# Performance work log

Hardware: AMD Instinct MI355X
Metric: run time of the kernel (lower is better)

Reference implementation:

```python
import jax, jax.numpy as jnp
import numpy as np

N, E, FS = 50000, 400000, 256
H, D = 8, 64            # GAT heads, hidden_size (per-head out_feats)
NH, DK, DV = 8, 64, 64  # transformer MHA
B = 1024
NEG_SLOPE = 0.2
EPS = 1e-6


def _layer_norm(x, g, b, eps=EPS):
    mu = x.mean(-1, keepdims=True)
    var = x.var(-1, keepdims=True)
    return (x - mu) / jnp.sqrt(var + eps) * g + b


def setup_inputs() -> dict:
    key = jax.random.key(0)
    ks = jax.random.split(key, 20)
    s = 0.02
    return {
        "features": jax.random.normal(ks[0], (N, FS), jnp.float32),
        "src": jax.random.randint(ks[1], (E,), 0, N, jnp.int32),
        "dst": jax.random.randint(ks[2], (E,), 0, N, jnp.int32),
        "url": jax.random.randint(ks[3], (B,), 1, N + 1, jnp.int32),  # 1-based ids
        # GATConv params (DGL-style)
        "gat_fc_w": jax.random.normal(ks[4], (FS, H * D), jnp.float32) * s,
        "attn_l": jax.random.normal(ks[5], (H, D), jnp.float32) * s,
        "attn_r": jax.random.normal(ks[6], (H, D), jnp.float32) * s,
        "gat_res_w": jax.random.normal(ks[7], (FS, H * D), jnp.float32) * s,
        "gat_bias": jnp.zeros((H, D), jnp.float32),
        # post-GAT LayerNorm
        "ln_g": jnp.ones((D,), jnp.float32),
        "ln_b": jnp.zeros((D,), jnp.float32),
        # MultiHeadAttention params
        "wq": jax.random.normal(ks[8], (D, NH * DK), jnp.float32) * s,
        "wk": jax.random.normal(ks[9], (D, NH * DK), jnp.float32) * s,
        "wv": jax.random.normal(ks[10], (D, NH * DV), jnp.float32) * s,
        "fc_w": jax.random.normal(ks[11], (NH * DV, D), jnp.float32) * s,
        "fc_b": jnp.zeros((D,), jnp.float32),
        "mha_ln_g": jnp.ones((D,), jnp.float32),
        "mha_ln_b": jnp.zeros((D,), jnp.float32),
        # final classifier
        "out_w": jax.random.normal(ks[12], (D, 2), jnp.float32) * s,
        "out_b": jnp.zeros((2,), jnp.float32),
    }


def reference(features, src, dst, url, gat_fc_w, attn_l, attn_r, gat_res_w,
              gat_bias, ln_g, ln_b, wq, wk, wv, fc_w, fc_b, mha_ln_g,
              mha_ln_b, out_w, out_b):
    # ---- GATConv (residual=True, bias, negative_slope=0.2, no activation) ----
    feat = (features @ gat_fc_w).reshape(N, H, D)          # [N,H,D]
    el = jnp.einsum('nhd,hd->nh', feat, attn_l)            # [N,H]
    er = jnp.einsum('nhd,hd->nh', feat, attn_r)            # [N,H]
    e = jax.nn.leaky_relu(el[src] + er[dst], NEG_SLOPE)    # [E,H] edge scores
    # segment softmax over incoming edges of each dst node
    m = jax.ops.segment_max(e, dst, num_segments=N)        # [N,H]
    m = jnp.where(jnp.isfinite(m), m, 0.0)
    ex = jnp.exp(e - m[dst])                               # [E,H]
    denom = jax.ops.segment_sum(ex, dst, num_segments=N)   # [N,H]
    a = ex / jnp.maximum(denom[dst], 1e-20)                # [E,H]
    msg = feat[src] * a[:, :, None]                        # [E,H,D]
    rst = jax.ops.segment_sum(msg, dst, num_segments=N)    # [N,H,D]
    res = (features @ gat_res_w).reshape(N, H, D)
    gat_emb = rst + res + gat_bias                         # [N,H,D]

    # ---- select batch nodes (url is 1-based) ----
    ids = url - 1
    x = gat_emb[ids]                                       # [B,H,D]
    x = _layer_norm(x, ln_g, ln_b)

    # ---- dense multi-head self-attention over the H gat heads (seq dim) ----
    residual = x
    q = (x @ wq).reshape(B, H, NH, DK)
    k = (x @ wk).reshape(B, H, NH, DK)
    v = (x @ wv).reshape(B, H, NH, DV)
    attn = jnp.einsum('bqhd,bkhd->bhqk', q, k) / jnp.sqrt(jnp.float32(DK))
    attn = jax.nn.softmax(attn, axis=-1)
    o = jnp.einsum('bhqk,bkhd->bqhd', attn, v).reshape(B, H, NH * DV)
    o = o @ fc_w + fc_b                                    # [B,H,D]
    o = _layer_norm(o + residual, mha_ln_g, mha_ln_b)

    # ---- pool + classify ----
    pooled = o.sum(axis=1)                                 # [B,D]
    logits = pooled @ out_w + out_b                        # [B,2]
    return logits
```

## Files before the change

### kernel.cpp

```cpp
#include <hip/hip_runtime.h>
#include <math.h>

#define Nn 50000
#define Ee 400000
#define FSz 256
#define HD_ 512
#define Bb 1024
#define HSZ 2048

static __device__ __forceinline__ int clampi(int v, int lo, int hi){
    return v < lo ? lo : (v > hi ? hi : v);
}
static __device__ __forceinline__ unsigned short f2bf(float f){
    unsigned int u = __float_as_uint(f);
    unsigned int r = u + 0x7FFFu + ((u >> 16) & 1u);
    return (unsigned short)(r >> 16);
}
static __device__ __forceinline__ float bflo(unsigned int v){ return __uint_as_float(v << 16); }
static __device__ __forceinline__ float bfhi(unsigned int v){ return __uint_as_float(v & 0xFFFF0000u); }

__global__ __launch_bounds__(256) void k_scatter(const int* __restrict__ src, const int* __restrict__ dst,
                                                 const int* __restrict__ url,
                                                 int* __restrict__ fill, int* __restrict__ slist,
                                                 const float* __restrict__ W,
                                                 const float* __restrict__ al,
                                                 const float* __restrict__ ar,
                                                 float* __restrict__ wl, float* __restrict__ wr){
    int t = threadIdx.x;
    if(blockIdx.x >= 1563){
        int bi = blockIdx.x - 1563;
        int wv = t >> 6, lane = t & 63;
        #pragma unroll
        for(int r = 0; r < 4; r++){
            int f = bi*16 + wv*4 + r;
            float pl[8], pr[8];
            #pragma unroll
            for(int h = 0; h < 8; h++){
                float w = W[f*512 + h*64 + lane];
                pl[h] = w * al[h*64 + lane];
                pr[h] = w * ar[h*64 + lane];
            }
            #pragma unroll
            for(int h = 0; h < 8; h++){
                #pragma unroll
                for(int m = 32; m >= 1; m >>= 1){
                    pl[h] += __shfl_xor(pl[h], m, 64);
                    pr[h] += __shfl_xor(pr[h], m, 64);
                }
            }
            #pragma unroll
            for(int h = 0; h < 8; h++){
                if(lane == h){ wl[h*256 + f] = pl[h]; wr[h*256 + f] = pr[h]; }
            }
        }
        return;
    }
    __shared__ int key[HSZ];
    __shared__ int chainhead[HSZ];
    __shared__ short nxt[Bb];
    for(int i = t; i < HSZ; i += 256){ key[i] = -1; chainhead[i] = -1; }
    __syncthreads();
    for(int b = t; b < Bb; b += 256){
        int n = clampi(url[b] - 1, 0, Nn - 1);
        int h = n & (HSZ - 1);
        while(true){
            int prev = atomicCAS(&key[h], -1, n);
            if(prev == -1 || prev == n) break;
            h = (h + 1) & (HSZ - 1);
        }
        int old = atomicExch(&chainhead[h], b);
        nxt[b] = (short)old;
    }
    __syncthreads();
    int e = blockIdx.x * 256 + t;
    if(e >= Ee) return;
    int d = dst[e];
    if((unsigned)d >= (unsigned)Nn) return;
    int h = d & (HSZ - 1);
    while(true){
        int k = key[h];
        if(k == -1) return;
        if(k == d) break;
        h = (h + 1) & (HSZ - 1);
    }
    int s = clampi(src[e], 0, Nn - 1);
    for(int b = chainhead[h]; b != -1; b = nxt[b]){
        int pos = atomicAdd(&fill[b], 1);
        if(pos < 64) slist[b*64 + pos] = s;
    }
}

__global__ __launch_bounds__(256) void k_gat(const float* __restrict__ features,
                                             const float* __restrict__ Wfc,
                                             const float* __restrict__ Wres,
                                             const float* __restrict__ bias,
                                             const float* __restrict__ wl,
                                             const float* __restrict__ wr,
                                             const int* __restrict__ url,
                                             const int* __restrict__ fill, const int* __restrict__ slist,
                                             float* __restrict__ gemb){
    int t = threadIdx.x;
    int lane = t & 63, wv = t >> 6;
    int u0 = blockIdx.x * 4;

    __shared__ float cxs[4][8][256];
    __shared__ float fres[4][256];
    __shared__ float sew[4][64][8];
    __shared__ float ser[4][8];
    __shared__ int   sslist[4][64];

    for(int i = t; i < 4*64*8; i += 256) ((float*)sew)[i] = 0.f;

    float4 rwl[8], rwr[8];
    #pragma unroll
    for(int h = 0; h < 8; h++){
        rwl[h] = *(const float4*)&wl[h*256 + 4*lane];
        rwr[h] = *(const float4*)&wr[h*256 + 4*lane];
    }

    int dg[4], nj[4];
    #pragma unroll
    for(int j = 0; j < 4; j++){
        int u = u0 + j;
        dg[j] = min(fill[u], 64);
        nj[j] = clampi(url[u] - 1, 0, Nn - 1);
        if(t < dg[j]) sslist[j][t] = slist[u*64 + t];
        fres[j][t] = features[(size_t)nj[j] * FSz + t];
    }
    __syncthreads();

    int c1 = dg[0], c2 = c1 + dg[1], c3 = c2 + dg[2];
    int total = c3 + dg[3];
    for(int tau = wv; tau < total + 4; tau += 4){
        int j, i, isEr = 0;
        if(tau < c1){ j = 0; i = tau; }
        else if(tau < c2){ j = 1; i = tau - c1; }
        else if(tau < c3){ j = 2; i = tau - c2; }
        else if(tau < total){ j = 3; i = tau - c3; }
        else { j = tau - total; i = 0; isEr = 1; }
        int s = isEr ? nj[j] : sslist[j][i];
        float4 x = *(const float4*)(features + (size_t)s * FSz + 4*lane);
        float p[8];
        if(isEr){
            #pragma unroll
            for(int h = 0; h < 8; h++)
                p[h] = x.x*rwr[h].x + x.y*rwr[h].y + x.z*rwr[h].z + x.w*rwr[h].w;
        } else {
            #pragma unroll
            for(int h = 0; h < 8; h++)
                p[h] = x.x*rwl[h].x + x.y*rwl[h].y + x.z*rwl[h].z + x.w*rwl[h].w;
        }
        #pragma unroll
        for(int h = 0; h < 8; h++){
            #pragma unroll
            for(int m = 32; m >= 1; m >>= 1) p[h] += __shfl_xor(p[h], m, 64);
        }
        if(lane == 0){
            if(isEr){
                #pragma unroll
                for(int h = 0; h < 8; h++) ser[j][h] = p[h];
            } else {
                #pragma unroll
                for(int h = 0; h < 8; h++) sew[j][i][h] = p[h];
            }
        }
    }
    __syncthreads();
    if(t < 32){
        int j = t >> 3, h = t & 7;
        int dgj = dg[j];
        if(dgj > 0){
            float ern = ser[j][h];
            float m = -1e30f;
            for(int i = 0; i < dgj; i++){
                float v = sew[j][i][h] + ern;
                v = v > 0.f ? v : 0.2f * v;
                m = fmaxf(m, v);
            }
            float sum = 0.f;
            for(int i = 0; i < dgj; i++){
                float v = sew[j][i][h] + ern;
                v = v > 0.f ? v : 0.2f * v;
                float w = expf(v - m);
                sum += w;
                sew[j][i][h] = w;
            }
            float inv = 1.0f / fmaxf(sum, 1e-20f);
            for(int i = 0; i < dgj; i++) sew[j][i][h] *= inv;
        }
    }
    __syncthreads();
    {
        float cx[4][8];
        #pragma unroll
        for(int j = 0; j < 4; j++)
            #pragma unroll
            for(int h = 0; h < 8; h++) cx[j][h] = 0.f;
        int mxd = max(max(dg[0], dg[1]), max(dg[2], dg[3]));
        for(int i = 0; i < mxd; i++){
            float x[4];
            #pragma unroll
            for(int j = 0; j < 4; j++){
                int s = (i < dg[j]) ? sslist[j][i] : 0;
                x[j] = features[(size_t)s * FSz + t];
            }
            #pragma unroll
            for(int j = 0; j < 4; j++){
                const float* av = &sew[j][i][0];
                float xm = (i < dg[j]) ? x[j] : 0.f;
                #pragma unroll
                for(int h = 0; h < 8; h++) cx[j][h] += av[h] * xm;
            }
        }
        #pragma unroll
        for(int j = 0; j < 4; j++)
            #pragma unroll
            for(int h = 0; h < 8; h++) cxs[j][h][t] = cx[j][h];
    }
    __syncthreads();

    int h = t >> 5;
    int o0 = 2 * t;
    const float2* Wfc2  = (const float2*)Wfc;
    const float2* Wres2 = (const float2*)Wres;
    float a[4][2] = {{0,0},{0,0},{0,0},{0,0}};
    for(int f = 0; f < 256; f += 4){
        float2 w0 = Wfc2[(f+0)*256 + t];
        float2 w1 = Wfc2[(f+1)*256 + t];
        float2 w2 = Wfc2[(f+2)*256 + t];
        float2 w3 = Wfc2[(f+3)*256 + t];
        float2 r0 = Wres2[(f+0)*256 + t];
        float2 r1 = Wres2[(f+1)*256 + t];
        float2 r2 = Wres2[(f+2)*256 + t];
        float2 r3 = Wres2[(f+3)*256 + t];
        #pragma unroll
        for(int j = 0; j < 4; j++){
            float4 c = *(const float4*)&cxs[j][h][f];
            float4 x = *(const float4*)&fres[j][f];
            a[j][0] += c.x*w0.x + c.y*w1.x + c.z*w2.x + c.w*w3.x
                     + x.x*r0.x + x.y*r1.x + x.z*r2.x + x.w*r3.x;
            a[j][1] += c.x*w0.y + c.y*w1.y + c.z*w2.y + c.w*w3.y
                     + x.x*r0.y + x.y*r1.y + x.z*r2.y + x.w*r3.y;
        }
    }
    float b0 = bias[o0], b1 = bias[o0 + 1];
    #pragma unroll
    for(int j = 0; j < 4; j++){
        float2* gp = (float2*)(gemb + (size_t)(u0 + j) * HD_);
        gp[t] = make_float2(a[j][0] + b0, a[j][1] + b1);
    }
}

__global__ __launch_bounds__(256, 2) void k_mha(const float* __restrict__ gemb,
                                             const float* __restrict__ lng, const float* __restrict__ lnb,
                                             const float* __restrict__ wq, const float* __restrict__ wk,
                                             const float* __restrict__ wvp, const float* __restrict__ fcw,
                                             const float* __restrict__ fcb, const float* __restrict__ mlg,
                                             const float* __restrict__ mlb, const float* __restrict__ outw,
                                             const float* __restrict__ outb, float* __restrict__ out){
    __shared__ float A[2][512];
    __shared__ float xnF[2][512];
    __shared__ unsigned short xnT[2][512];
    __shared__ unsigned short qkb[2][8320];
    __shared__ float mu8[2][8], rs8[2][8], pooled[2][64];

    int t = threadIdx.x;
    int lane = t & 63, wv = t >> 6;
    int e0 = blockIdx.x * 2;

    {
        const float* g0 = gemb + (size_t)e0 * HD_;
        const float* g1 = gemb + (size_t)(e0 + 1) * HD_;
        A[0][t] = g0[t]; A[0][t + 256] = g0[t + 256];
        A[1][t] = g1[t]; A[1][t + 256] = g1[t + 256];
    }
    __syncthreads();
    if(t < 16){
        int ee = t >> 3, q = t & 7;
        float s = 0.f, s2 = 0.f;
        for(int d = 0; d < 64; d++){ float v = A[ee][q*64 + d]; s += v; s2 += v * v; }
        float mu = s * (1.0f/64.0f);
        float var = s2 * (1.0f/64.0f) - mu * mu;
        mu8[ee][q] = mu; rs8[ee][q] = rsqrtf(fmaxf(var, 0.0f) + 1e-6f);
    }
    __syncthreads();
    #pragma unroll
    for(int p = 0; p < 4; p++){
        int i = p*256 + t; int ee = i >> 9, ii = i & 511, q = ii >> 6, d = ii & 63;
        float xv = (A[ee][ii] - mu8[ee][q]) * rs8[ee][q] * lng[d] + lnb[d];
        xnF[ee][ii] = xv;
        xnT[ee][d*8 + q] = f2bf(xv);
    }
    __syncthreads();
    float aq0[2][8], aq1[2][8], ak0[2][8], ak1[2][8], av0[2][8], av1[2][8];
    #pragma unroll
    for(int ee = 0; ee < 2; ee++)
        #pragma unroll
        for(int r = 0; r < 8; r++){
            aq0[ee][r]=0.f; aq1[ee][r]=0.f; ak0[ee][r]=0.f;
            ak1[ee][r]=0.f; av0[ee][r]=0.f; av1[ee][r]=0.f;
        }
    #pragma unroll 2
    for(int d = 0; d < 64; d++){
        float q0 = wq[d*512 + t],  q1 = wq[d*512 + t + 256];
        float k0 = wk[d*512 + t],  k1 = wk[d*512 + t + 256];
        float v0 = wvp[d*512 + t], v1 = wvp[d*512 + t + 256];
        #pragma unroll
        for(int ee = 0; ee < 2; ee++){
            uint4 xp = *(const uint4*)&xnT[ee][d*8];
            float xv[8] = { bflo(xp.x), bfhi(xp.x), bflo(xp.y), bfhi(xp.y),
                            bflo(xp.z), bfhi(xp.z), bflo(xp.w), bfhi(xp.w) };
            #pragma unroll
            for(int r = 0; r < 8; r++){
                aq0[ee][r] += xv[r]*q0; aq1[ee][r] += xv[r]*q1;
                ak0[ee][r] += xv[r]*k0; ak1[ee][r] += xv[r]*k1;
                av0[ee][r] += xv[r]*v0; av1[ee][r] += xv[r]*v1;
            }
        }
    }
    #pragma unroll
    for(int ee = 0; ee < 2; ee++)
        #pragma unroll
        for(int qq = 0; qq < 8; qq++){
            qkb[ee][qq*520 + t]              = f2bf(aq0[ee][qq]);
            qkb[ee][qq*520 + t + 256]        = f2bf(aq1[ee][qq]);
            qkb[ee][4160 + qq*520 + t]       = f2bf(ak0[ee][qq]);
            qkb[ee][4160 + qq*520 + t + 256] = f2bf(ak1[ee][qq]);
        }
    __syncthreads();
    #pragma unroll
    for(int p = 0; p < 4; p++){
        int i = p*256 + t;
        int ee = i >> 9, idx = i & 511;
        int nh = idx >> 6, qq = (idx >> 3) & 7, kk = idx & 7;
        const unsigned short* qrow = &qkb[ee][qq*520 + nh*64];
        const unsigned short* krow = &qkb[ee][4160 + kk*520 + nh*64];
        float s = 0.f;
        #pragma unroll
        for(int d8 = 0; d8 < 64; d8 += 8){
            uint4 qv = *(const uint4*)&qrow[d8];
            uint4 kv = *(const uint4*)&krow[d8];
            s += bflo(qv.x)*bflo(kv.x) + bfhi(qv.x)*bfhi(kv.x)
               + bflo(qv.y)*bflo(kv.y) + bfhi(qv.y)*bfhi(kv.y)
               + bflo(qv.z)*bflo(kv.z) + bfhi(qv.z)*bfhi(kv.z)
               + bflo(qv.w)*bflo(kv.w) + bfhi(qv.w)*bfhi(kv.w);
        }
        A[ee][idx] = s * 0.125f;
    }
    __syncthreads();
    if(t < 128){
        int ee = t >> 6, row = t & 63;
        float mx = -1e30f;
        #pragma unroll
        for(int k = 0; k < 8; k++) mx = fmaxf(mx, A[ee][row*8 + k]);
        float e[8]; float s = 0.f;
        #pragma unroll
        for(int k = 0; k < 8; k++){ e[k] = expf(A[ee][row*8 + k] - mx); s += e[k]; }
        float inv = 1.0f / s;
        #pragma unroll
        for(int k = 0; k < 8; k++) A[ee][row*8 + k] = e[k] * inv;
    }
    __syncthreads();
    {
        int nh0 = wv;
        #pragma unroll
        for(int ee = 0; ee < 2; ee++){
            #pragma unroll
            for(int qq = 0; qq < 8; qq++){
                const float* s0 = &A[ee][nh0*64 + qq*8];
                const float* s1 = &A[ee][(nh0+4)*64 + qq*8];
                float4 a0 = *(const float4*)s0, b0 = *(const float4*)(s0 + 4);
                float4 a1 = *(const float4*)s1, b1 = *(const float4*)(s1 + 4);
                float o0 = a0.x*av0[ee][0] + a0.y*av0[ee][1] + a0.z*av0[ee][2] + a0.w*av0[ee][3]
                         + b0.x*av0[ee][4] + b0.y*av0[ee][5] + b0.z*av0[ee][6] + b0.w*av0[ee][7];
                float o1 = a1.x*av1[ee][0] + a1.y*av1[ee][1] + a1.z*av1[ee][2] + a1.w*av1[ee][3]
                         + b1.x*av1[ee][4] + b1.y*av1[ee][5] + b1.z*av1[ee][6] + b1.w*av1[ee][7];
                qkb[ee][qq*520 + t]       = f2bf(o0);
                qkb[ee][qq*520 + t + 256] = f2bf(o1);
            }
        }
    }
    __syncthreads();
    {
        float* P0 = (float*)&qkb[0][4160];
        float* P1 = (float*)&qkb[1][4160];
        int g = lane & 31;
        int qh = lane >> 5;
        int k0r = wv * 128;
        float a[2][4][2];
        #pragma unroll
        for(int ee = 0; ee < 2; ee++)
            #pragma unroll
            for(int jq = 0; jq < 4; jq++){ a[ee][jq][0] = 0.f; a[ee][jq][1] = 0.f; }
        const float2* fw2 = (const float2*)fcw;
        for(int k = k0r; k < k0r + 128; k += 8){
            float2 f0 = fw2[(k+0)*32 + g];
            float2 f1 = fw2[(k+1)*32 + g];
            float2 f2 = fw2[(k+2)*32 + g];
            float2 f3 = fw2[(k+3)*32 + g];
            float2 f4 = fw2[(k+4)*32 + g];
            float2 f5 = fw2[(k+5)*32 + g];
            float2 f6 = fw2[(k+6)*32 + g];
            float2 f7 = fw2[(k+7)*32 + g];
            #pragma unroll
            for(int ee = 0; ee < 2; ee++){
                #pragma unroll
                for(int jq = 0; jq < 4; jq++){
                    int qq = qh*4 + jq;
                    uint4 op = *(const uint4*)&qkb[ee][qq*520 + k];
                    float x0 = bflo(op.x), x1 = bfhi(op.x), x2 = bflo(op.y), x3 = bfhi(op.y);
                    float x4 = bflo(op.z), x5 = bfhi(op.z), x6 = bflo(op.w), x7 = bfhi(op.w);
                    a[ee][jq][0] += x0*f0.x + x1*f1.x + x2*f2.x + x3*f3.x + x4*f4.x + x5*f5.x + x6*f6.x + x7*f7.x;
                    a[ee][jq][1] += x0*f0.y + x1*f1.y + x2*f2.y + x3*f3.y + x4*f4.y + x5*f5.y + x6*f6.y + x7*f7.y;
                }
            }
        }
        __syncthreads();
        #pragma unroll
        for(int jq = 0; jq < 4; jq++){
            int qq = qh*4 + jq;
            *(float2*)&P0[wv*512 + qq*64 + 2*g] = make_float2(a[0][jq][0], a[0][jq][1]);
            *(float2*)&P1[wv*512 + qq*64 + 2*g] = make_float2(a[1][jq][0], a[1][jq][1]);
        }
        __syncthreads();
        #pragma unroll
        for(int p = 0; p < 4; p++){
            int i = p*256 + t;
            int ee = i >> 9, o = i & 511, dd = o & 63;
            const float* P = ee ? P1 : P0;
            A[ee][o] = P[o] + P[512 + o] + P[1024 + o] + P[1536 + o] + fcb[dd] + xnF[ee][o];
        }
    }
    __syncthreads();
    if(t < 16){
        int ee = t >> 3, q = t & 7;
        float s = 0.f, s2 = 0.f;
        for(int d = 0; d < 64; d++){ float v = A[ee][q*64 + d]; s += v; s2 += v * v; }
        float mu = s * (1.0f/64.0f);
        float var = s2 * (1.0f/64.0f) - mu * mu;
        mu8[ee][q] = mu; rs8[ee][q] = rsqrtf(fmaxf(var, 0.0f) + 1e-6f);
    }
    __syncthreads();
    if(t < 128){
        int ee = t >> 6, dd = t & 63;
        float g2 = mlg[dd], bb = mlb[dd];
        float s = 0.f;
        #pragma unroll
        for(int qq = 0; qq < 8; qq++)
            s += (A[ee][qq*64 + dd] - mu8[ee][qq]) * rs8[ee][qq] * g2 + bb;
        pooled[ee][dd] = s;
    }
    __syncthreads();
    if(t < 4){
        int ee = t >> 1, c = t & 1;
        float s = outb[c];
        for(int d = 0; d < 64; d++) s += pooled[ee][d] * outw[d*2 + c];
        out[(e0 + ee)*2 + c] = s;
    }
}

extern "C" void kernel_launch(void* const* d_in, const int* in_sizes, int n_in,
                              void* d_out, int out_size, void* d_ws, size_t ws_size,
                              hipStream_t stream){
    (void)in_sizes; (void)n_in; (void)out_size; (void)ws_size;
    const float* features  = (const float*)d_in[0];
    const int*   src       = (const int*)d_in[1];
    const int*   dst       = (const int*)d_in[2];
    const int*   url       = (const int*)d_in[3];
    const float* gat_fc_w  = (const float*)d_in[4];
    const float* attn_l    = (const float*)d_in[5];
    const float* attn_r    = (const float*)d_in[6];
    const float* gat_res_w = (const float*)d_in[7];
    const float* gat_bias  = (const float*)d_in[8];
    const float* ln_g      = (const float*)d_in[9];
    const float* ln_b      = (const float*)d_in[10];
    const float* wq        = (const float*)d_in[11];
    const float* wk        = (const float*)d_in[12];
    const float* wv        = (const float*)d_in[13];
    const float* fc_w      = (const float*)d_in[14];
    const float* fc_b      = (const float*)d_in[15];
    const float* mha_ln_g  = (const float*)d_in[16];
    const float* mha_ln_b  = (const float*)d_in[17];
    const float* out_w     = (const float*)d_in[18];
    const float* out_b     = (const float*)d_in[19];

    char* base = (char*)d_ws;
    size_t cur = 0;
    auto alloc = [&](size_t nbytes) -> void* {
        void* p = base + cur;
        cur = (cur + nbytes + 255) & ~(size_t)255;
        return p;
    };
    float* wl    = (float*)alloc(2048 * sizeof(float));
    float* wr    = (float*)alloc(2048 * sizeof(float));
    int*   fill  = (int*)alloc(1024 * sizeof(int));
    int*   slist = (int*)alloc((size_t)1024 * 64 * sizeof(int));
    float* gemb  = (float*)alloc((size_t)1024 * 512 * sizeof(float));

    hipMemsetAsync(fill, 0, 1024 * sizeof(int), stream);

    hipLaunchKernelGGL(k_scatter, dim3(1579), dim3(256), 0, stream, src, dst, url, fill, slist,
                       gat_fc_w, attn_l, attn_r, wl, wr);
    hipLaunchKernelGGL(k_gat,     dim3(256),  dim3(256), 0, stream, features, gat_fc_w, gat_res_w, gat_bias,
                       wl, wr, url, fill, slist, gemb);
    hipLaunchKernelGGL(k_mha,     dim3(512),  dim3(256), 0, stream, gemb, ln_g, ln_b,
                       wq, wk, wv, fc_w, fc_b, mha_ln_g, mha_ln_b, out_w, out_b,
                       (float*)d_out);
}
```

Baseline: 210.7 us.

## Halve nodes per GAT block and double MHA block threads

k_gat now handles 2 batch nodes per block instead of 4 and launches 512 blocks, so 256 CUs get more blocks and parallelism. Its neighbour aggregation loop is also unrolled by 2 to keep more gathers in flight. k_mha moves from 256 to 512 threads per block, so each thread owns one output column instead of two, and the fc stage splits across both batch elements by warp. The cost is that each fetched weight row is reused across fewer nodes in k_gat, and per-block register and sync pressure rises in k_mha.

```diff
diff --git a/kernel.cpp b/kernel.cpp
--- a/kernel.cpp
+++ b/kernel.cpp
@@ -101,15 +101,15 @@
                                              float* __restrict__ gemb){
     int t = threadIdx.x;
     int lane = t & 63, wv = t >> 6;
-    int u0 = blockIdx.x * 4;
-
-    __shared__ float cxs[4][8][256];
-    __shared__ float fres[4][256];
-    __shared__ float sew[4][64][8];
-    __shared__ float ser[4][8];
-    __shared__ int   sslist[4][64];
-
-    for(int i = t; i < 4*64*8; i += 256) ((float*)sew)[i] = 0.f;
+    int u0 = blockIdx.x * 2;
+
+    __shared__ float cxs[2][8][256];
+    __shared__ float fres[2][256];
+    __shared__ float sew[2][64][8];
+    __shared__ float ser[2][8];
+    __shared__ int   sslist[2][64];
+
+    for(int i = t; i < 2*64*8; i += 256) ((float*)sew)[i] = 0.f;
 
     float4 rwl[8], rwr[8];
     #pragma unroll
@@ -118,9 +118,9 @@
         rwr[h] = *(const float4*)&wr[h*256 + 4*lane];
     }
 
-    int dg[4], nj[4];
-    #pragma unroll
-    for(int j = 0; j < 4; j++){
+    int dg[2], nj[2];
+    #pragma unroll
+    for(int j = 0; j < 2; j++){
         int u = u0 + j;
         dg[j] = min(fill[u], 64);
         nj[j] = clampi(url[u] - 1, 0, Nn - 1);
@@ -129,14 +129,12 @@
     }
     __syncthreads();
 
-    int c1 = dg[0], c2 = c1 + dg[1], c3 = c2 + dg[2];
-    int total = c3 + dg[3];
-    for(int tau = wv; tau < total + 4; tau += 4){
+    int c1 = dg[0];
+    int total = c1 + dg[1];
+    for(int tau = wv; tau < total + 2; tau += 4){
         int j, i, isEr = 0;
         if(tau < c1){ j = 0; i = tau; }
-        else if(tau < c2){ j = 1; i = tau - c1; }
-        else if(tau < c3){ j = 2; i = tau - c2; }
-        else if(tau < total){ j = 3; i = tau - c3; }
+        else if(tau < total){ j = 1; i = tau - c1; }
         else { j = tau - total; i = 0; isEr = 1; }
         int s = isEr ? nj[j] : sslist[j][i];
         float4 x = *(const float4*)(features + (size_t)s * FSz + 4*lane);
@@ -166,7 +164,7 @@
         }
     }
     __syncthreads();
-    if(t < 32){
+    if(t < 16){
         int j = t >> 3, h = t & 7;
         int dgj = dg[j];
         if(dgj > 0){
@@ -191,29 +189,35 @@
     }
     __syncthreads();
     {
-        float cx[4][8];
-        #pragma unroll
-        for(int j = 0; j < 4; j++)
+        float cx[2][8];
+        #pragma unroll
+        for(int j = 0; j < 2; j++)
             #pragma unroll
             for(int h = 0; h < 8; h++) cx[j][h] = 0.f;
-        int mxd = max(max(dg[0], dg[1]), max(dg[2], dg[3]));
-        for(int i = 0; i < mxd; i++){
-            float x[4];
-            #pragma unroll
-            for(int j = 0; j < 4; j++){
-                int s = (i < dg[j]) ? sslist[j][i] : 0;
-                x[j] = features[(size_t)s * FSz + t];
-            }
-            #pragma unroll
-            for(int j = 0; j < 4; j++){
-                const float* av = &sew[j][i][0];
-                float xm = (i < dg[j]) ? x[j] : 0.f;
+        int mxd = max(dg[0], dg[1]);
+        for(int i = 0; i < mxd; i += 2){
+            float x[2][2];
+            #pragma unroll
+            for(int j = 0; j < 2; j++)
                 #pragma unroll
-                for(int h = 0; h < 8; h++) cx[j][h] += av[h] * xm;
-            }
-        }
-        #pragma unroll
-        for(int j = 0; j < 4; j++)
+                for(int ii = 0; ii < 2; ii++){
+                    int idx = i + ii;
+                    int s = (idx < dg[j]) ? sslist[j][idx] : 0;
+                    x[j][ii] = features[(size_t)s * FSz + t];
+                }
+            #pragma unroll
+            for(int j = 0; j < 2; j++)
+                #pragma unroll
+                for(int ii = 0; ii < 2; ii++){
+                    int idx = i + ii;
+                    const float* av = &sew[j][idx < 64 ? idx : 0][0];
+                    float xm = (idx < dg[j]) ? x[j][ii] : 0.f;
+                    #pragma unroll
+                    for(int h = 0; h < 8; h++) cx[j][h] += av[h] * xm;
+                }
+        }
+        #pragma unroll
+        for(int j = 0; j < 2; j++)
             #pragma unroll
             for(int h = 0; h < 8; h++) cxs[j][h][t] = cx[j][h];
     }
@@ -223,7 +227,7 @@
     int o0 = 2 * t;
     const float2* Wfc2  = (const float2*)Wfc;
     const float2* Wres2 = (const float2*)Wres;
-    float a[4][2] = {{0,0},{0,0},{0,0},{0,0}};
+    float a[2][2] = {{0,0},{0,0}};
     for(int f = 0; f < 256; f += 4){
         float2 w0 = Wfc2[(f+0)*256 + t];
         float2 w1 = Wfc2[(f+1)*256 + t];
@@ -234,7 +238,7 @@
         float2 r2 = Wres2[(f+2)*256 + t];
         float2 r3 = Wres2[(f+3)*256 + t];
         #pragma unroll
-        for(int j = 0; j < 4; j++){
+        for(int j = 0; j < 2; j++){
             float4 c = *(const float4*)&cxs[j][h][f];
             float4 x = *(const float4*)&fres[j][f];
             a[j][0] += c.x*w0.x + c.y*w1.x + c.z*w2.x + c.w*w3.x
@@ -245,13 +249,13 @@
     }
     float b0 = bias[o0], b1 = bias[o0 + 1];
     #pragma unroll
-    for(int j = 0; j < 4; j++){
+    for(int j = 0; j < 2; j++){
         float2* gp = (float2*)(gemb + (size_t)(u0 + j) * HD_);
         gp[t] = make_float2(a[j][0] + b0, a[j][1] + b1);
     }
 }
 
-__global__ __launch_bounds__(256, 2) void k_mha(const float* __restrict__ gemb,
+__global__ __launch_bounds__(512, 2) void k_mha(const float* __restrict__ gemb,
                                              const float* __restrict__ lng, const float* __restrict__ lnb,
                                              const float* __restrict__ wq, const float* __restrict__ wk,
                                              const float* __restrict__ wvp, const float* __restrict__ fcw,
@@ -271,8 +275,8 @@
     {
         const float* g0 = gemb + (size_t)e0 * HD_;
         const float* g1 = gemb + (size_t)(e0 + 1) * HD_;
-        A[0][t] = g0[t]; A[0][t + 256] = g0[t + 256];
-        A[1][t] = g1[t]; A[1][t + 256] = g1[t + 256];
+        A[0][t] = g0[t];
+        A[1][t] = g1[t];
     }
     __syncthreads();
     if(t < 16){
@@ -285,26 +289,23 @@
     }
     __syncthreads();
     #pragma unroll
-    for(int p = 0; p < 4; p++){
-        int i = p*256 + t; int ee = i >> 9, ii = i & 511, q = ii >> 6, d = ii & 63;
+    for(int p = 0; p < 2; p++){
+        int i = p*512 + t; int ee = i >> 9, ii = i & 511, q = ii >> 6, d = ii & 63;
         float xv = (A[ee][ii] - mu8[ee][q]) * rs8[ee][q] * lng[d] + lnb[d];
         xnF[ee][ii] = xv;
         xnT[ee][d*8 + q] = f2bf(xv);
     }
     __syncthreads();
-    float aq0[2][8], aq1[2][8], ak0[2][8], ak1[2][8], av0[2][8], av1[2][8];
+    float aq[2][8], ak[2][8], av[2][8];
     #pragma unroll
     for(int ee = 0; ee < 2; ee++)
         #pragma unroll
-        for(int r = 0; r < 8; r++){
-            aq0[ee][r]=0.f; aq1[ee][r]=0.f; ak0[ee][r]=0.f;
-            ak1[ee][r]=0.f; av0[ee][r]=0.f; av1[ee][r]=0.f;
-        }
+        for(int r = 0; r < 8; r++){ aq[ee][r]=0.f; ak[ee][r]=0.f; av[ee][r]=0.f; }
     #pragma unroll 2
     for(int d = 0; d < 64; d++){
-        float q0 = wq[d*512 + t],  q1 = wq[d*512 + t + 256];
-        float k0 = wk[d*512 + t],  k1 = wk[d*512 + t + 256];
-        float v0 = wvp[d*512 + t], v1 = wvp[d*512 + t + 256];
+        float q0 = wq[d*512 + t];
+        float k0 = wk[d*512 + t];
+        float v0 = wvp[d*512 + t];
         #pragma unroll
         for(int ee = 0; ee < 2; ee++){
             uint4 xp = *(const uint4*)&xnT[ee][d*8];
@@ -312,9 +313,9 @@
                             bflo(xp.z), bfhi(xp.z), bflo(xp.w), bfhi(xp.w) };
             #pragma unroll
             for(int r = 0; r < 8; r++){
-                aq0[ee][r] += xv[r]*q0; aq1[ee][r] += xv[r]*q1;
-                ak0[ee][r] += xv[r]*k0; ak1[ee][r] += xv[r]*k1;
-                av0[ee][r] += xv[r]*v0; av1[ee][r] += xv[r]*v1;
+                aq[ee][r] += xv[r]*q0;
+                ak[ee][r] += xv[r]*k0;
+                av[ee][r] += xv[r]*v0;
             }
         }
     }
@@ -322,15 +323,13 @@
     for(int ee = 0; ee < 2; ee++)
         #pragma unroll
         for(int qq = 0; qq < 8; qq++){
-            qkb[ee][qq*520 + t]              = f2bf(aq0[ee][qq]);
-            qkb[ee][qq*520 + t + 256]        = f2bf(aq1[ee][qq]);
-            qkb[ee][4160 + qq*520 + t]       = f2bf(ak0[ee][qq]);
-            qkb[ee][4160 + qq*520 + t + 256] = f2bf(ak1[ee][qq]);
-        }
-    __syncthreads();
-    #pragma unroll
-    for(int p = 0; p < 4; p++){
-        int i = p*256 + t;
+            qkb[ee][qq*520 + t]        = f2bf(aq[ee][qq]);
+            qkb[ee][4160 + qq*520 + t] = f2bf(ak[ee][qq]);
+        }
+    __syncthreads();
+    #pragma unroll
+    for(int p = 0; p < 2; p++){
+        int i = p*512 + t;
         int ee = i >> 9, idx = i & 511;
         int nh = idx >> 6, qq = (idx >> 3) & 7, kk = idx & 7;
         const unsigned short* qrow = &qkb[ee][qq*520 + nh*64];
@@ -362,21 +361,16 @@
     }
     __syncthreads();
     {
-        int nh0 = wv;
+        int nh = t >> 6;
         #pragma unroll
         for(int ee = 0; ee < 2; ee++){
             #pragma unroll
             for(int qq = 0; qq < 8; qq++){
-                const float* s0 = &A[ee][nh0*64 + qq*8];
-                const float* s1 = &A[ee][(nh0+4)*64 + qq*8];
+                const float* s0 = &A[ee][nh*64 + qq*8];
                 float4 a0 = *(const float4*)s0, b0 = *(const float4*)(s0 + 4);
-                float4 a1 = *(const float4*)s1, b1 = *(const float4*)(s1 + 4);
-                float o0 = a0.x*av0[ee][0] + a0.y*av0[ee][1] + a0.z*av0[ee][2] + a0.w*av0[ee][3]
-                         + b0.x*av0[ee][4] + b0.y*av0[ee][5] + b0.z*av0[ee][6] + b0.w*av0[ee][7];
-                float o1 = a1.x*av1[ee][0] + a1.y*av1[ee][1] + a1.z*av1[ee][2] + a1.w*av1[ee][3]
-                         + b1.x*av1[ee][4] + b1.y*av1[ee][5] + b1.z*av1[ee][6] + b1.w*av1[ee][7];
-                qkb[ee][qq*520 + t]       = f2bf(o0);
-                qkb[ee][qq*520 + t + 256] = f2bf(o1);
+                float o0 = a0.x*av[ee][0] + a0.y*av[ee][1] + a0.z*av[ee][2] + a0.w*av[ee][3]
+                         + b0.x*av[ee][4] + b0.y*av[ee][5] + b0.z*av[ee][6] + b0.w*av[ee][7];
+                qkb[ee][qq*520 + t] = f2bf(o0);
             }
         }
     }
@@ -384,14 +378,11 @@
     {
         float* P0 = (float*)&qkb[0][4160];
         float* P1 = (float*)&qkb[1][4160];
+        int ee = wv >> 2;
+        int k0r = (wv & 3) * 128;
         int g = lane & 31;
         int qh = lane >> 5;
-        int k0r = wv * 128;
-        float a[2][4][2];
-        #pragma unroll
-        for(int ee = 0; ee < 2; ee++)
-            #pragma unroll
-            for(int jq = 0; jq < 4; jq++){ a[ee][jq][0] = 0.f; a[ee][jq][1] = 0.f; }
+        float a[4][2] = {{0,0},{0,0},{0,0},{0,0}};
         const float2* fw2 = (const float2*)fcw;
         for(int k = k0r; k < k0r + 128; k += 8){
             float2 f0 = fw2[(k+0)*32 + g];
@@ -403,32 +394,31 @@
             float2 f6 = fw2[(k+6)*32 + g];
             float2 f7 = fw2[(k+7)*32 + g];
             #pragma unroll
-            for(int ee = 0; ee < 2; ee++){
-                #pragma unroll
-                for(int jq = 0; jq < 4; jq++){
-                    int qq = qh*4 + jq;
-                    uint4 op = *(const uint4*)&qkb[ee][qq*520 + k];
-                    float x0 = bflo(op.x), x1 = bfhi(op.x), x2 = bflo(op.y), x3 = bfhi(op.y);
-                    float x4 = bflo(op.z), x5 = bfhi(op.z), x6 = bflo(op.w), x7 = bfhi(op.w);
-                    a[ee][jq][0] += x0*f0.x + x1*f1.x + x2*f2.x + x3*f3.x + x4*f4.x + x5*f5.x + x6*f6.x + x7*f7.x;
-                    a[ee][jq][1] += x0*f0.y + x1*f1.y + x2*f2.y + x3*f3.y + x4*f4.y + x5*f5.y + x6*f6.y + x7*f7.y;
-                }
+            for(int jq = 0; jq < 4; jq++){
+                int qq = qh*4 + jq;
+                uint4 op = *(const uint4*)&qkb[ee][qq*520 + k];
+                float x0 = bflo(op.x), x1 = bfhi(op.x), x2 = bflo(op.y), x3 = bfhi(op.y);
+                float x4 = bflo(op.z), x5 = bfhi(op.z), x6 = bflo(op.w), x7 = bfhi(op.w);
+                a[jq][0] += x0*f0.x + x1*f1.x + x2*f2.x + x3*f3.x + x4*f4.x + x5*f5.x + x6*f6.x + x7*f7.x;
+                a[jq][1] += x0*f0.y + x1*f1.y + x2*f2.y + x3*f3.y + x4*f4.y + x5*f5.y + x6*f6.y + x7*f7.y;
             }
         }
         __syncthreads();
-        #pragma unroll
-        for(int jq = 0; jq < 4; jq++){
-            int qq = qh*4 + jq;
-            *(float2*)&P0[wv*512 + qq*64 + 2*g] = make_float2(a[0][jq][0], a[0][jq][1]);
-            *(float2*)&P1[wv*512 + qq*64 + 2*g] = make_float2(a[1][jq][0], a[1][jq][1]);
+        {
+            float* P = ee ? P1 : P0;
+            #pragma unroll
+            for(int jq = 0; jq < 4; jq++){
+                int qq = qh*4 + jq;
+                *(float2*)&P[(wv & 3)*512 + qq*64 + 2*g] = make_float2(a[jq][0], a[jq][1]);
+            }
         }
         __syncthreads();
         #pragma unroll
-        for(int p = 0; p < 4; p++){
-            int i = p*256 + t;
-            int ee = i >> 9, o = i & 511, dd = o & 63;
-            const float* P = ee ? P1 : P0;
-            A[ee][o] = P[o] + P[512 + o] + P[1024 + o] + P[1536 + o] + fcb[dd] + xnF[ee][o];
+        for(int p = 0; p < 2; p++){
+            int i = p*512 + t;
+            int e2 = i >> 9, o = i & 511, dd = o & 63;
+            const float* P = e2 ? P1 : P0;
+            A[e2][o] = P[o] + P[512 + o] + P[1024 + o] + P[1536 + o] + fcb[dd] + xnF[e2][o];
         }
     }
     __syncthreads();
@@ -501,9 +491,9 @@
 
     hipLaunchKernelGGL(k_scatter, dim3(1579), dim3(256), 0, stream, src, dst, url, fill, slist,
                        gat_fc_w, attn_l, attn_r, wl, wr);
-    hipLaunchKernelGGL(k_gat,     dim3(256),  dim3(256), 0, stream, features, gat_fc_w, gat_res_w, gat_bias,
+    hipLaunchKernelGGL(k_gat,     dim3(512),  dim3(256), 0, stream, features, gat_fc_w, gat_res_w, gat_bias,
                        wl, wr, url, fill, slist, gemb);
-    hipLaunchKernelGGL(k_mha,     dim3(512),  dim3(256), 0, stream, gemb, ln_g, ln_b,
+    hipLaunchKernelGGL(k_mha,     dim3(512),  dim3(512), 0, stream, gemb, ln_g, ln_b,
                        wq, wk, wv, fc_w, fc_b, mha_ln_g, mha_ln_b, out_w, out_b,
                        (float*)d_out);
 }
```

New measurement: 216.5 us. 2.7% more time.

## Convert GAT weights to bf16 and halve nodes per block in k_gat

Applied to the files above, without the earlier changes.

The scatter kernel gains 32 extra blocks that convert the fc and residual weight matrices to packed bf16. k_gat now processes 2 batch nodes per block instead of 4, doubling the grid to 512 blocks, and unrolls the neighbor aggregation loop by 2. The intent is to halve weight read bandwidth in the projection stage and to improve occupancy and memory-level parallelism. In exchange, weights are re-read twice as often across blocks, and bf16 weights lose precision.

```diff
diff --git a/kernel.cpp b/kernel.cpp
--- a/kernel.cpp
+++ b/kernel.cpp
@@ -25,8 +25,26 @@
                                                  const float* __restrict__ W,
                                                  const float* __restrict__ al,
                                                  const float* __restrict__ ar,
-                                                 float* __restrict__ wl, float* __restrict__ wr){
+                                                 float* __restrict__ wl, float* __restrict__ wr,
+                                                 const float* __restrict__ Wfc,
+                                                 const float* __restrict__ Wres,
+                                                 unsigned int* __restrict__ wfcb,
+                                                 unsigned int* __restrict__ wresb){
     int t = threadIdx.x;
+    if(blockIdx.x >= 1579){
+        int bi = blockIdx.x - 1579;
+        int m = bi >> 4;
+        const float2* Sf = (const float2*)(m ? Wres : Wfc);
+        unsigned int* D = m ? wresb : wfcb;
+        int base = (bi & 15) * 8192;
+        #pragma unroll
+        for(int i = 0; i < 32; i++){
+            int idx = base + i*256 + t;
+            float2 v = Sf[idx];
+            D[idx] = ((unsigned int)f2bf(v.y) << 16) | (unsigned int)f2bf(v.x);
+        }
+        return;
+    }
     if(blockIdx.x >= 1563){
         int bi = blockIdx.x - 1563;
         int wv = t >> 6, lane = t & 63;
@@ -91,8 +109,8 @@
 }
 
 __global__ __launch_bounds__(256) void k_gat(const float* __restrict__ features,
-                                             const float* __restrict__ Wfc,
-                                             const float* __restrict__ Wres,
+                                             const unsigned int* __restrict__ Wfcb,
+                                             const unsigned int* __restrict__ Wresb,
                                              const float* __restrict__ bias,
                                              const float* __restrict__ wl,
                                              const float* __restrict__ wr,
@@ -101,15 +119,15 @@
                                              float* __restrict__ gemb){
     int t = threadIdx.x;
     int lane = t & 63, wv = t >> 6;
-    int u0 = blockIdx.x * 4;
-
-    __shared__ float cxs[4][8][256];
-    __shared__ float fres[4][256];
-    __shared__ float sew[4][64][8];
-    __shared__ float ser[4][8];
-    __shared__ int   sslist[4][64];
-
-    for(int i = t; i < 4*64*8; i += 256) ((float*)sew)[i] = 0.f;
+    int u0 = blockIdx.x * 2;
+
+    __shared__ float cxs[2][8][256];
+    __shared__ float fres[2][256];
+    __shared__ float sew[2][64][8];
+    __shared__ float ser[2][8];
+    __shared__ int   sslist[2][64];
+
+    for(int i = t; i < 2*64*8; i += 256) ((float*)sew)[i] = 0.f;
 
     float4 rwl[8], rwr[8];
     #pragma unroll
@@ -118,9 +136,9 @@
         rwr[h] = *(const float4*)&wr[h*256 + 4*lane];
     }
 
-    int dg[4], nj[4];
-    #pragma unroll
-    for(int j = 0; j < 4; j++){
+    int dg[2], nj[2];
+    #pragma unroll
+    for(int j = 0; j < 2; j++){
         int u = u0 + j;
         dg[j] = min(fill[u], 64);
         nj[j] = clampi(url[u] - 1, 0, Nn - 1);
@@ -129,14 +147,12 @@
     }
     __syncthreads();
 
-    int c1 = dg[0], c2 = c1 + dg[1], c3 = c2 + dg[2];
-    int total = c3 + dg[3];
-    for(int tau = wv; tau < total + 4; tau += 4){
+    int c1 = dg[0];
+    int total = c1 + dg[1];
+    for(int tau = wv; tau < total + 2; tau += 4){
         int j, i, isEr = 0;
         if(tau < c1){ j = 0; i = tau; }
-        else if(tau < c2){ j = 1; i = tau - c1; }
-        else if(tau < c3){ j = 2; i = tau - c2; }
-        else if(tau < total){ j = 3; i = tau - c3; }
+        else if(tau < total){ j = 1; i = tau - c1; }
         else { j = tau - total; i = 0; isEr = 1; }
         int s = isEr ? nj[j] : sslist[j][i];
         float4 x = *(const float4*)(features + (size_t)s * FSz + 4*lane);
@@ -166,7 +182,7 @@
         }
     }
     __syncthreads();
-    if(t < 32){
+    if(t < 16){
         int j = t >> 3, h = t & 7;
         int dgj = dg[j];
         if(dgj > 0){
@@ -191,29 +207,35 @@
     }
     __syncthreads();
     {
-        float cx[4][8];
-        #pragma unroll
-        for(int j = 0; j < 4; j++)
+        float cx[2][8];
+        #pragma unroll
+        for(int j = 0; j < 2; j++)
             #pragma unroll
             for(int h = 0; h < 8; h++) cx[j][h] = 0.f;
-        int mxd = max(max(dg[0], dg[1]), max(dg[2], dg[3]));
-        for(int i = 0; i < mxd; i++){
-            float x[4];
-            #pragma unroll
-            for(int j = 0; j < 4; j++){
-                int s = (i < dg[j]) ? sslist[j][i] : 0;
-                x[j] = features[(size_t)s * FSz + t];
-            }
-            #pragma unroll
-            for(int j = 0; j < 4; j++){
-                const float* av = &sew[j][i][0];
-                float xm = (i < dg[j]) ? x[j] : 0.f;
+        int mxd = max(dg[0], dg[1]);
+        for(int i = 0; i < mxd; i += 2){
+            float x[2][2];
+            #pragma unroll
+            for(int j = 0; j < 2; j++)
                 #pragma unroll
-                for(int h = 0; h < 8; h++) cx[j][h] += av[h] * xm;
-            }
-        }
-        #pragma unroll
-        for(int j = 0; j < 4; j++)
+                for(int ii = 0; ii < 2; ii++){
+                    int idx = i + ii;
+                    int s = (idx < dg[j]) ? sslist[j][idx] : 0;
+                    x[j][ii] = features[(size_t)s * FSz + t];
+                }
+            #pragma unroll
+            for(int j = 0; j < 2; j++)
+                #pragma unroll
+                for(int ii = 0; ii < 2; ii++){
+                    int idx = i + ii;
+                    const float* av = &sew[j][idx < 64 ? idx : 0][0];
+                    float xm = (idx < dg[j]) ? x[j][ii] : 0.f;
+                    #pragma unroll
+                    for(int h = 0; h < 8; h++) cx[j][h] += av[h] * xm;
+                }
+        }
+        #pragma unroll
+        for(int j = 0; j < 2; j++)
             #pragma unroll
             for(int h = 0; h < 8; h++) cxs[j][h][t] = cx[j][h];
     }
@@ -221,31 +243,29 @@
 
     int h = t >> 5;
     int o0 = 2 * t;
-    const float2* Wfc2  = (const float2*)Wfc;
-    const float2* Wres2 = (const float2*)Wres;
-    float a[4][2] = {{0,0},{0,0},{0,0},{0,0}};
+    float a[2][2] = {{0,0},{0,0}};
     for(int f = 0; f < 256; f += 4){
-        float2 w0 = Wfc2[(f+0)*256 + t];
-        float2 w1 = Wfc2[(f+1)*256 + t];
-        float2 w2 = Wfc2[(f+2)*256 + t];
-        float2 w3 = Wfc2[(f+3)*256 + t];
-        float2 r0 = Wres2[(f+0)*256 + t];
-        float2 r1 = Wres2[(f+1)*256 + t];
-        float2 r2 = Wres2[(f+2)*256 + t];
-        float2 r3 = Wres2[(f+3)*256 + t];
-        #pragma unroll
-        for(int j = 0; j < 4; j++){
+        unsigned int w0 = Wfcb[(f+0)*256 + t];
+        unsigned int w1 = Wfcb[(f+1)*256 + t];
+        unsigned int w2 = Wfcb[(f+2)*256 + t];
+        unsigned int w3 = Wfcb[(f+3)*256 + t];
+        unsigned int r0 = Wresb[(f+0)*256 + t];
+        unsigned int r1 = Wresb[(f+1)*256 + t];
+        unsigned int r2 = Wresb[(f+2)*256 + t];
+        unsigned int r3 = Wresb[(f+3)*256 + t];
+        #pragma unroll
+        for(int j = 0; j < 2; j++){
             float4 c = *(const float4*)&cxs[j][h][f];
             float4 x = *(const float4*)&fres[j][f];
-            a[j][0] += c.x*w0.x + c.y*w1.x + c.z*w2.x + c.w*w3.x
-                     + x.x*r0.x + x.y*r1.x + x.z*r2.x + x.w*r3.x;
-            a[j][1] += c.x*w0.y + c.y*w1.y + c.z*w2.y + c.w*w3.y
-                     + x.x*r0.y + x.y*r1.y + x.z*r2.y + x.w*r3.y;
+            a[j][0] += c.x*bflo(w0) + c.y*bflo(w1) + c.z*bflo(w2) + c.w*bflo(w3)
+                     + x.x*bflo(r0) + x.y*bflo(r1) + x.z*bflo(r2) + x.w*bflo(r3);
+            a[j][1] += c.x*bfhi(w0) + c.y*bfhi(w1) + c.z*bfhi(w2) + c.w*bfhi(w3)
+                     + x.x*bfhi(r0) + x.y*bfhi(r1) + x.z*bfhi(r2) + x.w*bfhi(r3);
         }
     }
     float b0 = bias[o0], b1 = bias[o0 + 1];
     #pragma unroll
-    for(int j = 0; j < 4; j++){
+    for(int j = 0; j < 2; j++){
         float2* gp = (float2*)(gemb + (size_t)(u0 + j) * HD_);
         gp[t] = make_float2(a[j][0] + b0, a[j][1] + b1);
     }
@@ -491,17 +511,19 @@
         cur = (cur + nbytes + 255) & ~(size_t)255;
         return p;
     };
-    float* wl    = (float*)alloc(2048 * sizeof(float));
-    float* wr    = (float*)alloc(2048 * sizeof(float));
-    int*   fill  = (int*)alloc(1024 * sizeof(int));
-    int*   slist = (int*)alloc((size_t)1024 * 64 * sizeof(int));
-    float* gemb  = (float*)alloc((size_t)1024 * 512 * sizeof(float));
+    float*        wl    = (float*)alloc(2048 * sizeof(float));
+    float*        wr    = (float*)alloc(2048 * sizeof(float));
+    int*          fill  = (int*)alloc(1024 * sizeof(int));
+    int*          slist = (int*)alloc((size_t)1024 * 64 * sizeof(int));
+    float*        gemb  = (float*)alloc((size_t)1024 * 512 * sizeof(float));
+    unsigned int* wfcb  = (unsigned int*)alloc((size_t)256 * 512 * sizeof(unsigned short));
+    unsigned int* wresb = (unsigned int*)alloc((size_t)256 * 512 * sizeof(unsigned short));
 
     hipMemsetAsync(fill, 0, 1024 * sizeof(int), stream);
 
-    hipLaunchKernelGGL(k_scatter, dim3(1579), dim3(256), 0, stream, src, dst, url, fill, slist,
-                       gat_fc_w, attn_l, attn_r, wl, wr);
-    hipLaunchKernelGGL(k_gat,     dim3(256),  dim3(256), 0, stream, features, gat_fc_w, gat_res_w, gat_bias,
+    hipLaunchKernelGGL(k_scatter, dim3(1611), dim3(256), 0, stream, src, dst, url, fill, slist,
+                       gat_fc_w, attn_l, attn_r, wl, wr, gat_fc_w, gat_res_w, wfcb, wresb);
+    hipLaunchKernelGGL(k_gat,     dim3(512),  dim3(256), 0, stream, features, wfcb, wresb, gat_bias,
                        wl, wr, url, fill, slist, gemb);
     hipLaunchKernelGGL(k_mha,     dim3(512),  dim3(256), 0, stream, gemb, ln_g, ln_b,
                        wq, wk, wv, fc_w, fc_b, mha_ln_g, mha_ln_b, out_w, out_b,
```

After: 203.4 us. -3.5%, faster.
